# Optimization experiments

Measured on AMD Instinct MI355X. Metric: run time of the kernel, lower is better.

Reference implementation:

```python
import jax, jax.numpy as jnp
import numpy as np

N_LAYERS = 4  # n_layer + 1 in the torch module

def setup_inputs() -> dict:
    key = jax.random.key(0)
    k1, k2, k3 = jax.random.split(key, 3)
    B, F = 32768, 1024
    x = jax.random.normal(k1, (B, F), dtype=jnp.float32)
    Ws = jax.random.normal(k2, (N_LAYERS, F), dtype=jnp.float32)
    Bs = jax.random.normal(k3, (N_LAYERS, F), dtype=jnp.float32)
    return {"x": x, "Ws": Ws, "Bs": Bs}

def reference(x, Ws, Bs):
    # Cross layer: x_{i+1} = x0 * (x_i^T w_i) + b_i + x_i
    # (matmul(x0 x_i^T, w_i) == x0 * dot(x_i, w_i) -- same math, O(n) form)
    x0 = x
    xi = x
    for i in range(N_LAYERS):
        s = jnp.einsum('bf,f->b', xi, Ws[i])      # [B] per-sample dot product
        xi = x0 * s[:, None] + Bs[i][None, :] + xi  # [B, F]
    return xi
```

## Files before the change

### kernel.cpp

```cpp
#include <hip/hip_runtime.h>

#define FDIM 1024
#define NLAYERS 4

typedef float v4f __attribute__((ext_vector_type(4)));

__global__ __launch_bounds__(256) void cross_net_kernel(
    const float* __restrict__ x, const float* __restrict__ Ws,
    const float* __restrict__ Bs, float* __restrict__ out, int nrows) {
  const int wave = threadIdx.x >> 6;
  const int lane = threadIdx.x & 63;
  const int row = blockIdx.x * 4 + wave;
  if (row >= nrows) return;

  const float* xr = x + (size_t)row * FDIM;
  v4f x0[4], xi[4];
#pragma unroll
  for (int c = 0; c < 4; ++c) {
    x0[c] = __builtin_nontemporal_load(
        reinterpret_cast<const v4f*>(xr + c * 256 + lane * 4));
    xi[c] = x0[c];
  }

#pragma unroll
  for (int i = 0; i < NLAYERS; ++i) {
    const float* W = Ws + i * FDIM;
    const float* B = Bs + i * FDIM;
    v4f w[4], b[4];
#pragma unroll
    for (int c = 0; c < 4; ++c) {
      w[c] = *reinterpret_cast<const v4f*>(W + c * 256 + lane * 4);
      b[c] = *reinterpret_cast<const v4f*>(B + c * 256 + lane * 4);
    }
    float s = 0.f;
#pragma unroll
    for (int c = 0; c < 4; ++c) {
      s = fmaf(xi[c].x, w[c].x, s);
      s = fmaf(xi[c].y, w[c].y, s);
      s = fmaf(xi[c].z, w[c].z, s);
      s = fmaf(xi[c].w, w[c].w, s);
    }
#pragma unroll
    for (int off = 32; off > 0; off >>= 1) s += __shfl_xor(s, off, 64);
#pragma unroll
    for (int c = 0; c < 4; ++c) {
      xi[c].x = fmaf(x0[c].x, s, b[c].x + xi[c].x);
      xi[c].y = fmaf(x0[c].y, s, b[c].y + xi[c].y);
      xi[c].z = fmaf(x0[c].z, s, b[c].z + xi[c].z);
      xi[c].w = fmaf(x0[c].w, s, b[c].w + xi[c].w);
    }
  }

  float* outr = out + (size_t)row * FDIM;
#pragma unroll
  for (int c = 0; c < 4; ++c)
    __builtin_nontemporal_store(
        xi[c], reinterpret_cast<v4f*>(outr + c * 256 + lane * 4));
}

extern "C" void kernel_launch(void* const* d_in, const int* in_sizes, int n_in,
                              void* d_out, int out_size, void* d_ws, size_t ws_size,
                              hipStream_t stream) {
  const float* x  = (const float*)d_in[0];
  const float* Ws = (const float*)d_in[1];
  const float* Bs = (const float*)d_in[2];
  float* out = (float*)d_out;
  const int nrows = in_sizes[0] / FDIM;
  const int grid = (nrows + 3) / 4;
  hipLaunchKernelGGL(cross_net_kernel, dim3(grid), dim3(256), 0, stream,
                     x, Ws, Bs, out, nrows);
}
```

Before: 249.7 us.

## Rewrite cross layers in closed form with precomputed bias terms

```diff
diff --git a/kernel.cpp b/kernel.cpp
--- a/kernel.cpp
+++ b/kernel.cpp
@@ -5,57 +5,97 @@
 
 typedef float v4f __attribute__((ext_vector_type(4)));
 
-__global__ __launch_bounds__(256) void cross_net_kernel(
+
+__global__ __launch_bounds__(256) void cross_net_pre(
+    const float* __restrict__ Ws, const float* __restrict__ Bs,
+    float* __restrict__ ws) {
+  const int t = threadIdx.x;
+  __shared__ float red[3][256];
+  float e1 = 0.f, e2 = 0.f, e3 = 0.f;
+#pragma unroll
+  for (int c = 0; c < 4; ++c) {
+    const int f = c * 256 + t;
+    const float B0 = Bs[0 * FDIM + f], B1 = Bs[1 * FDIM + f];
+    const float B2 = Bs[2 * FDIM + f], B3 = Bs[3 * FDIM + f];
+    const float W1 = Ws[1 * FDIM + f], W2 = Ws[2 * FDIM + f];
+    const float W3 = Ws[3 * FDIM + f];
+    const float beta1 = B0;
+    const float beta2 = beta1 + B1;
+    const float beta3 = beta2 + B2;
+    e1 = fmaf(beta1, W1, e1);
+    e2 = fmaf(beta2, W2, e2);
+    e3 = fmaf(beta3, W3, e3);
+    ws[16 + f] = beta3 + B3;
+  }
+  red[0][t] = e1; red[1][t] = e2; red[2][t] = e3;
+  __syncthreads();
+#pragma unroll
+  for (int s = 128; s > 0; s >>= 1) {
+    if (t < s) {
+      red[0][t] += red[0][t + s];
+      red[1][t] += red[1][t + s];
+      red[2][t] += red[2][t + s];
+    }
+    __syncthreads();
+  }
+  if (t == 0) { ws[0] = red[0][0]; ws[1] = red[1][0]; ws[2] = red[2][0]; }
+}
+
+__global__ __launch_bounds__(256) void cross_net_main(
     const float* __restrict__ x, const float* __restrict__ Ws,
-    const float* __restrict__ Bs, float* __restrict__ out, int nrows) {
+    const float* __restrict__ ws, float* __restrict__ out, int nrows) {
   const int wave = threadIdx.x >> 6;
   const int lane = threadIdx.x & 63;
   const int row = blockIdx.x * 4 + wave;
   if (row >= nrows) return;
 
   const float* xr = x + (size_t)row * FDIM;
-  v4f x0[4], xi[4];
+  v4f x0[4];
 #pragma unroll
-  for (int c = 0; c < 4; ++c) {
+  for (int c = 0; c < 4; ++c)
     x0[c] = __builtin_nontemporal_load(
         reinterpret_cast<const v4f*>(xr + c * 256 + lane * 4));
-    xi[c] = x0[c];
-  }
 
+  float d[4];
 #pragma unroll
-  for (int i = 0; i < NLAYERS; ++i) {
-    const float* W = Ws + i * FDIM;
-    const float* B = Bs + i * FDIM;
-    v4f w[4], b[4];
-#pragma unroll
-    for (int c = 0; c < 4; ++c) {
-      w[c] = *reinterpret_cast<const v4f*>(W + c * 256 + lane * 4);
-      b[c] = *reinterpret_cast<const v4f*>(B + c * 256 + lane * 4);
-    }
+  for (int j = 0; j < NLAYERS; ++j) {
+    const float* W = Ws + j * FDIM;
     float s = 0.f;
 #pragma unroll
     for (int c = 0; c < 4; ++c) {
-      s = fmaf(xi[c].x, w[c].x, s);
-      s = fmaf(xi[c].y, w[c].y, s);
-      s = fmaf(xi[c].z, w[c].z, s);
-      s = fmaf(xi[c].w, w[c].w, s);
+      const v4f w = *reinterpret_cast<const v4f*>(W + c * 256 + lane * 4);
+      s = fmaf(x0[c].x, w.x, s);
+      s = fmaf(x0[c].y, w.y, s);
+      s = fmaf(x0[c].z, w.z, s);
+      s = fmaf(x0[c].w, w.w, s);
     }
+    d[j] = s;
+  }
 #pragma unroll
-    for (int off = 32; off > 0; off >>= 1) s += __shfl_xor(s, off, 64);
+  for (int off = 32; off > 0; off >>= 1) {
 #pragma unroll
-    for (int c = 0; c < 4; ++c) {
-      xi[c].x = fmaf(x0[c].x, s, b[c].x + xi[c].x);
-      xi[c].y = fmaf(x0[c].y, s, b[c].y + xi[c].y);
-      xi[c].z = fmaf(x0[c].z, s, b[c].z + xi[c].z);
-      xi[c].w = fmaf(x0[c].w, s, b[c].w + xi[c].w);
-    }
+    for (int j = 0; j < NLAYERS; ++j) d[j] += __shfl_xor(d[j], off, 64);
   }
 
+  const float e1 = ws[0], e2 = ws[1], e3 = ws[2];
+  float a = 1.f + d[0];
+  a += fmaf(a, d[1], e1);
+  a += fmaf(a, d[2], e2);
+  a += fmaf(a, d[3], e3);
+
+  const float* SB = ws + 16;
   float* outr = out + (size_t)row * FDIM;
 #pragma unroll
-  for (int c = 0; c < 4; ++c)
+  for (int c = 0; c < 4; ++c) {
+    const v4f sb = *reinterpret_cast<const v4f*>(SB + c * 256 + lane * 4);
+    v4f r;
+    r.x = fmaf(a, x0[c].x, sb.x);
+    r.y = fmaf(a, x0[c].y, sb.y);
+    r.z = fmaf(a, x0[c].z, sb.z);
+    r.w = fmaf(a, x0[c].w, sb.w);
     __builtin_nontemporal_store(
-        xi[c], reinterpret_cast<v4f*>(outr + c * 256 + lane * 4));
+        r, reinterpret_cast<v4f*>(outr + c * 256 + lane * 4));
+  }
 }
 
 extern "C" void kernel_launch(void* const* d_in, const int* in_sizes, int n_in,
@@ -65,8 +105,10 @@
   const float* Ws = (const float*)d_in[1];
   const float* Bs = (const float*)d_in[2];
   float* out = (float*)d_out;
+  float* ws  = (float*)d_ws;
   const int nrows = in_sizes[0] / FDIM;
+  hipLaunchKernelGGL(cross_net_pre, dim3(1), dim3(256), 0, stream, Ws, Bs, ws);
   const int grid = (nrows + 3) / 4;
-  hipLaunchKernelGGL(cross_net_kernel, dim3(grid), dim3(256), 0, stream,
-                     x, Ws, Bs, out, nrows);
+  hipLaunchKernelGGL(cross_net_main, dim3(grid), dim3(256), 0, stream,
+                     x, Ws, ws, out, nrows);
 }
```

Measured after the change: 238.3 us, median of 2. -4.6%, faster.

## Collapse cross layers into a single scalar recurrence with one batched reduction

Applied to the files above, without the earlier changes.

```diff
diff --git a/kernel.cpp b/kernel.cpp
--- a/kernel.cpp
+++ b/kernel.cpp
@@ -5,7 +5,8 @@
 
 typedef float v4f __attribute__((ext_vector_type(4)));
 
-__global__ __launch_bounds__(256) void cross_net_kernel(
+
+__global__ __launch_bounds__(256) void cross_net_fused(
     const float* __restrict__ x, const float* __restrict__ Ws,
     const float* __restrict__ Bs, float* __restrict__ out, int nrows) {
   const int wave = threadIdx.x >> 6;
@@ -14,48 +15,79 @@
   if (row >= nrows) return;
 
   const float* xr = x + (size_t)row * FDIM;
-  v4f x0[4], xi[4];
+  v4f x0[4];
+#pragma unroll
+  for (int c = 0; c < 4; ++c)
+    x0[c] = __builtin_nontemporal_load(
+        reinterpret_cast<const v4f*>(xr + c * 256 + lane * 4));
+
+  float d0 = 0.f, d1 = 0.f, d2 = 0.f, d3 = 0.f;
+  float e1 = 0.f, e2 = 0.f, e3 = 0.f;
+  v4f sb[4];
+
 #pragma unroll
   for (int c = 0; c < 4; ++c) {
-    x0[c] = __builtin_nontemporal_load(
-        reinterpret_cast<const v4f*>(xr + c * 256 + lane * 4));
-    xi[c] = x0[c];
+    const int off = c * 256 + lane * 4;
+    const v4f b0 = *reinterpret_cast<const v4f*>(Bs + 0 * FDIM + off);
+    const v4f b1 = *reinterpret_cast<const v4f*>(Bs + 1 * FDIM + off);
+    const v4f b2 = *reinterpret_cast<const v4f*>(Bs + 2 * FDIM + off);
+    const v4f b3 = *reinterpret_cast<const v4f*>(Bs + 3 * FDIM + off);
+    const v4f beta1 = b0;
+    const v4f beta2 = beta1 + b1;
+    const v4f beta3 = beta2 + b2;
+    sb[c] = beta3 + b3;
+
+    const v4f w0 = *reinterpret_cast<const v4f*>(Ws + 0 * FDIM + off);
+    const v4f w1 = *reinterpret_cast<const v4f*>(Ws + 1 * FDIM + off);
+    const v4f w2 = *reinterpret_cast<const v4f*>(Ws + 2 * FDIM + off);
+    const v4f w3 = *reinterpret_cast<const v4f*>(Ws + 3 * FDIM + off);
+
+    d0 = fmaf(x0[c].x, w0.x, d0); d0 = fmaf(x0[c].y, w0.y, d0);
+    d0 = fmaf(x0[c].z, w0.z, d0); d0 = fmaf(x0[c].w, w0.w, d0);
+
+    d1 = fmaf(x0[c].x, w1.x, d1); d1 = fmaf(x0[c].y, w1.y, d1);
+    d1 = fmaf(x0[c].z, w1.z, d1); d1 = fmaf(x0[c].w, w1.w, d1);
+    e1 = fmaf(beta1.x, w1.x, e1); e1 = fmaf(beta1.y, w1.y, e1);
+    e1 = fmaf(beta1.z, w1.z, e1); e1 = fmaf(beta1.w, w1.w, e1);
+
+    d2 = fmaf(x0[c].x, w2.x, d2); d2 = fmaf(x0[c].y, w2.y, d2);
+    d2 = fmaf(x0[c].z, w2.z, d2); d2 = fmaf(x0[c].w, w2.w, d2);
+    e2 = fmaf(beta2.x, w2.x, e2); e2 = fmaf(beta2.y, w2.y, e2);
+    e2 = fmaf(beta2.z, w2.z, e2); e2 = fmaf(beta2.w, w2.w, e2);
+
+    d3 = fmaf(x0[c].x, w3.x, d3); d3 = fmaf(x0[c].y, w3.y, d3);
+    d3 = fmaf(x0[c].z, w3.z, d3); d3 = fmaf(x0[c].w, w3.w, d3);
+    e3 = fmaf(beta3.x, w3.x, e3); e3 = fmaf(beta3.y, w3.y, e3);
+    e3 = fmaf(beta3.z, w3.z, e3); e3 = fmaf(beta3.w, w3.w, e3);
   }
 
 #pragma unroll
-  for (int i = 0; i < NLAYERS; ++i) {
-    const float* W = Ws + i * FDIM;
-    const float* B = Bs + i * FDIM;
-    v4f w[4], b[4];
-#pragma unroll
-    for (int c = 0; c < 4; ++c) {
-      w[c] = *reinterpret_cast<const v4f*>(W + c * 256 + lane * 4);
-      b[c] = *reinterpret_cast<const v4f*>(B + c * 256 + lane * 4);
-    }
-    float s = 0.f;
-#pragma unroll
-    for (int c = 0; c < 4; ++c) {
-      s = fmaf(xi[c].x, w[c].x, s);
-      s = fmaf(xi[c].y, w[c].y, s);
-      s = fmaf(xi[c].z, w[c].z, s);
-      s = fmaf(xi[c].w, w[c].w, s);
-    }
-#pragma unroll
-    for (int off = 32; off > 0; off >>= 1) s += __shfl_xor(s, off, 64);
-#pragma unroll
-    for (int c = 0; c < 4; ++c) {
-      xi[c].x = fmaf(x0[c].x, s, b[c].x + xi[c].x);
-      xi[c].y = fmaf(x0[c].y, s, b[c].y + xi[c].y);
-      xi[c].z = fmaf(x0[c].z, s, b[c].z + xi[c].z);
-      xi[c].w = fmaf(x0[c].w, s, b[c].w + xi[c].w);
-    }
+  for (int off = 32; off > 0; off >>= 1) {
+    d0 += __shfl_xor(d0, off, 64);
+    d1 += __shfl_xor(d1, off, 64);
+    d2 += __shfl_xor(d2, off, 64);
+    d3 += __shfl_xor(d3, off, 64);
+    e1 += __shfl_xor(e1, off, 64);
+    e2 += __shfl_xor(e2, off, 64);
+    e3 += __shfl_xor(e3, off, 64);
   }
+
+  float a = 1.f + d0;
+  a += fmaf(a, d1, e1);
+  a += fmaf(a, d2, e2);
+  a += fmaf(a, d3, e3);
 
   float* outr = out + (size_t)row * FDIM;
 #pragma unroll
-  for (int c = 0; c < 4; ++c)
+  for (int c = 0; c < 4; ++c) {
+    v4f r;
+    r.x = fmaf(a, x0[c].x, sb[c].x);
+    r.y = fmaf(a, x0[c].y, sb[c].y);
+    r.z = fmaf(a, x0[c].z, sb[c].z);
+    r.w = fmaf(a, x0[c].w, sb[c].w);
     __builtin_nontemporal_store(
-        xi[c], reinterpret_cast<v4f*>(outr + c * 256 + lane * 4));
+        r, reinterpret_cast<v4f*>(outr + c * 256 + lane * 4));
+  }
 }
 
 extern "C" void kernel_launch(void* const* d_in, const int* in_sizes, int n_in,
@@ -67,6 +99,6 @@
   float* out = (float*)d_out;
   const int nrows = in_sizes[0] / FDIM;
   const int grid = (nrows + 3) / 4;
-  hipLaunchKernelGGL(cross_net_kernel, dim3(grid), dim3(256), 0, stream,
+  hipLaunchKernelGGL(cross_net_fused, dim3(grid), dim3(256), 0, stream,
                      x, Ws, Bs, out, nrows);
 }
```

Result: no change. 248.3 us (-0.6%).
